# Kernel tuning notes

Hardware: AMD Instinct MI355X
Metric: run time of the kernel (lower is better)

## Reference

```python
import jax, jax.numpy as jnp
import numpy as np

G, K_ORD = 5, 3          # efficient-kan defaults: grid_size=5, spline_order=3
NB = G + K_ORD           # 8 spline basis functions per input feature
H, NH, S, B = 1024, 16, 1024, 2
HD = H // NH
DFF, E, TOPK = 1024, 4, 2


def b_splines(x):
    # x: [..., in] -> bases: [..., in, NB]; uniform grid on [-1,1] extended by K_ORD knots
    h = 2.0 / G
    grid = jnp.arange(-K_ORD, G + K_ORD + 1, dtype=x.dtype) * h - 1.0  # [G+2k+1]=12
    xg = x[..., None]
    bases = ((xg >= grid[:-1]) & (xg < grid[1:])).astype(x.dtype)      # order-0
    for j in range(1, K_ORD + 1):  # Cox-de Boor recursion
        left = (xg - grid[:-(j + 1)]) / (grid[j:-1] - grid[:-(j + 1)]) * bases[..., :-1]
        right = (grid[j + 1:] - xg) / (grid[j + 1:] - grid[1:-j]) * bases[..., 1:]
        bases = left + right
    return bases  # [..., in, NB]


def kan_linear(x, base_w, spline_w, scaler):
    # base path: SiLU(x) @ W_base^T ; spline path: B(x) contracted with scaled spline weights
    base = jax.nn.silu(x) @ base_w.T                       # [..., out]
    sw = spline_w * scaler[..., None]                      # [out, in, NB]
    spline = jnp.einsum('...ic,oic->...o', b_splines(x), sw)
    return base + spline


def rmsnorm(x, w, eps=1e-6):
    return w * (x * jax.lax.rsqrt(jnp.mean(x * x, axis=-1, keepdims=True) + eps))


def ffn(x, b1, s1, c1, b2, s2, c2, b3, s3, c3):
    # linear3(linear1(x) * linear2(x)), all KANLinear
    return kan_linear(kan_linear(x, b1, s1, c1) * kan_linear(x, b2, s2, c2), b3, s3, c3)


def setup_inputs() -> dict:
    key = jax.random.key(0)
    ks = jax.random.split(key, 24)
    sc = 0.02
    d = {}
    d['x'] = jax.random.normal(ks[0], (B, S, H), jnp.float32)
    inv_freq = 1.0 / (10000.0 ** (np.arange(0, HD, 2, dtype=np.float32) / HD))
    ang = np.arange(S, dtype=np.float32)[:, None] * inv_freq[None, :]  # [S, HD//2]
    d['rot_cos'] = jnp.asarray(np.cos(ang))
    d['rot_sin'] = jnp.asarray(np.sin(ang))
    d['norm1_w'] = jnp.ones((H,), jnp.float32)
    d['norm2_w'] = jnp.ones((H,), jnp.float32)
    d['qkv_base'] = jax.random.normal(ks[1], (3 * H, H), jnp.float32) * sc
    d['qkv_spline'] = jax.random.normal(ks[2], (3 * H, H, NB), jnp.float32) * sc
    d['qkv_scaler'] = jax.random.normal(ks[3], (3 * H, H), jnp.float32) * sc + 1.0
    d['out_w'] = jax.random.normal(ks[4], (H, H), jnp.float32) * sc
    d['out_b'] = jnp.zeros((H,), jnp.float32)
    d['gate_w'] = jax.random.normal(ks[5], (E, H), jnp.float32) * sc
    # stacked expert params (vmapped over E)
    d['w1_base'] = jax.random.normal(ks[6], (E, DFF, H), jnp.float32) * sc
    d['w1_spline'] = jax.random.normal(ks[7], (E, DFF, H, NB), jnp.float32) * sc
    d['w1_scaler'] = jax.random.normal(ks[8], (E, DFF, H), jnp.float32) * sc + 1.0
    d['w2_base'] = jax.random.normal(ks[9], (E, DFF, H), jnp.float32) * sc
    d['w2_spline'] = jax.random.normal(ks[10], (E, DFF, H, NB), jnp.float32) * sc
    d['w2_scaler'] = jax.random.normal(ks[11], (E, DFF, H), jnp.float32) * sc + 1.0
    d['w3_base'] = jax.random.normal(ks[12], (E, H, DFF), jnp.float32) * sc
    d['w3_spline'] = jax.random.normal(ks[13], (E, H, DFF, NB), jnp.float32) * sc
    d['w3_scaler'] = jax.random.normal(ks[14], (E, H, DFF), jnp.float32) * sc + 1.0
    return d


def reference(x, rot_cos, rot_sin, norm1_w, norm2_w, qkv_base, qkv_spline, qkv_scaler,
              out_w, out_b, gate_w, w1_base, w1_spline, w1_scaler, w2_base, w2_spline,
              w2_scaler, w3_base, w3_spline, w3_scaler):
    b, s, h = x.shape
    # ---- attention branch ----
    hn = rmsnorm(x, norm1_w)
    qkv = kan_linear(hn, qkv_base, qkv_spline, qkv_scaler)          # [B,S,3H]
    qkv = qkv.reshape(b, s, NH, 3 * HD).transpose(0, 2, 1, 3)       # [B,NH,S,3HD]
    q, k, v = jnp.split(qkv, 3, axis=-1)                            # [B,NH,S,HD]

    def rope(t):
        tr = t.reshape(b, NH, s, HD // 2, 2)
        re, im = tr[..., 0], tr[..., 1]
        c, sn = rot_cos[:s], rot_sin[:s]                            # [S,HD//2]
        nre = re * c - im * sn
        nim = re * sn + im * c
        return jnp.stack([nre, nim], axis=-1).reshape(b, NH, s, HD)

    q, k = rope(q), rope(k)
    scores = jnp.einsum('bhqd,bhkd->bhqk', q, k) / (HD ** 0.5)
    attn = jax.nn.softmax(scores, axis=-1)
    ctx = jnp.einsum('bhqk,bhkd->bhqd', attn, v)
    ctx = ctx.transpose(0, 2, 1, 3).reshape(b, s, h)
    x = x + ctx @ out_w.T + out_b

    # ---- MoE-KAN FFN branch ----
    h2 = rmsnorm(x, norm2_w)
    gate_logits = h2 @ gate_w.T                                     # [B,S,E]
    w_top, sel = jax.lax.top_k(gate_logits, TOPK)                   # [B,S,K]
    w_top = jax.nn.softmax(w_top.astype(jnp.float32), axis=-1).astype(x.dtype)
    # run every expert densely (same math as masked dispatch), then gather top-k
    y_all = jax.vmap(
        lambda b1, s1, c1, b2, s2, c2, b3, s3, c3:
            ffn(h2, b1, s1, c1, b2, s2, c2, b3, s3, c3)
    )(w1_base, w1_spline, w1_scaler, w2_base, w2_spline, w2_scaler,
      w3_base, w3_spline, w3_scaler)                                # [E,B,S,H]
    y_bseh = jnp.transpose(y_all, (1, 2, 0, 3))                     # [B,S,E,H]
    gathered = jnp.take_along_axis(y_bseh, sel[..., None], axis=2)  # [B,S,K,H]
    moe_out = jnp.sum(w_top[..., None] * gathered, axis=2)          # [B,S,H]
    return x + moe_out
```

## Files before the change

### kernel.cpp

```cpp
#include <hip/hip_runtime.h>
#include <hip/hip_bf16.h>

#define T_TOK 2048
#define H_DIM 1024
#define S_SEQ 1024
#define NHEAD 16
#define E_EXP 4
#define DFF_  1024
#define KAUG  9216

typedef __bf16 bf16x8 __attribute__((ext_vector_type(8)));
typedef float  f32x4  __attribute__((ext_vector_type(4)));
typedef unsigned short ushort_t;

__device__ __forceinline__ float sigmoidf_(float x) { return 1.0f / (1.0f + __expf(-x)); }

__device__ __forceinline__ unsigned short f2bf(float f) {
    unsigned int u = __float_as_uint(f);
    u = (u + 0x7fffu + ((u >> 16) & 1u)) >> 16;
    return (unsigned short)u;
}
__device__ __forceinline__ float bf2f(unsigned short h) {
    return __uint_as_float(((unsigned int)h) << 16);
}

__device__ __forceinline__ void bspline8(float x, float* o) {
    float b[11];
#pragma unroll
    for (int m = 0; m < 11; ++m) {
        float g0 = 0.4f * (float)(m - 3) - 1.0f;
        float g1 = 0.4f * (float)(m - 2) - 1.0f;
        b[m] = (x >= g0 && x < g1) ? 1.0f : 0.0f;
    }
#pragma unroll
    for (int j = 1; j <= 3; ++j) {
        float inv = 1.0f / (0.4f * (float)j);
#pragma unroll
        for (int m = 0; m + j < 11; ++m) {
            float gm   = 0.4f * (float)(m - 3) - 1.0f;
            float gmj1 = 0.4f * (float)(m + j - 2) - 1.0f;
            b[m] = ((x - gm) * b[m] + (gmj1 - x) * b[m + 1]) * inv;
        }
    }
#pragma unroll
    for (int c = 0; c < 8; ++c) o[c] = b[c];
}

__global__ __launch_bounds__(256) void rmsnorm_kernel(const float* __restrict__ x,
                                                      const float* __restrict__ w,
                                                      float* __restrict__ out) {
    long t = blockIdx.x;
    float4 v = ((const float4*)(x + t * H_DIM))[threadIdx.x];
    float ss = v.x * v.x + v.y * v.y + v.z * v.z + v.w * v.w;
#pragma unroll
    for (int m = 1; m < 64; m <<= 1) ss += __shfl_xor(ss, m, 64);
    __shared__ float wsum[4];
    if ((threadIdx.x & 63) == 0) wsum[threadIdx.x >> 6] = ss;
    __syncthreads();
    ss = wsum[0] + wsum[1] + wsum[2] + wsum[3];
    float sc = rsqrtf(ss * (1.0f / (float)H_DIM) + 1e-6f);
    float4 wv = ((const float4*)w)[threadIdx.x];
    float4 r;
    r.x = v.x * sc * wv.x; r.y = v.y * sc * wv.y;
    r.z = v.z * sc * wv.z; r.w = v.w * sc * wv.w;
    ((float4*)(out + t * H_DIM))[threadIdx.x] = r;
}

__global__ __launch_bounds__(256) void prefill_out(const float* __restrict__ x,
                                                   const float* __restrict__ bias,
                                                   float* __restrict__ out) {
    long i = (long)blockIdx.x * 256 + threadIdx.x;
    float4 xv = ((const float4*)x)[i];
    float4 bv = ((const float4*)bias)[i & 255];
    float4 r;
    r.x = xv.x + bv.x; r.y = xv.y + bv.y; r.z = xv.z + bv.z; r.w = xv.w + bv.w;
    ((float4*)out)[i] = r;
}

__global__ __launch_bounds__(256) void pack_act(const float* __restrict__ act,
                                                ushort_t* __restrict__ hi,
                                                ushort_t* __restrict__ lo) {
    long idx = (long)blockIdx.x * 256 + threadIdx.x;
    long m = idx >> 10; int i = (int)(idx & 1023);
    float v = act[idx];
    float ch[9];
    ch[0] = v * sigmoidf_(v);
    bspline8(v, ch + 1);
    ushort_t* oh = hi + m * (long)KAUG + i;
#pragma unroll
    for (int c = 0; c < 9; ++c) oh[(long)c * 1024] = f2bf(ch[c]);
    if (lo) {
        ushort_t* ol = lo + m * (long)KAUG + i;
#pragma unroll
        for (int c = 0; c < 9; ++c) {
            unsigned short h = f2bf(ch[c]);
            ol[(long)c * 1024] = f2bf(ch[c] - bf2f(h));
        }
    }
}

__global__ __launch_bounds__(256) void pack_w(const float* __restrict__ base,
                                              const float* __restrict__ spl,
                                              const float* __restrict__ scal,
                                              ushort_t* __restrict__ hi,
                                              ushort_t* __restrict__ lo,
                                              long total) {
    long idx = (long)blockIdx.x * 256 + threadIdx.x;
    if (idx >= total) return;
    long n = idx >> 10; int i = (int)(idx & 1023);
    float sc = scal[idx];
    const float4* s4 = (const float4*)(spl + idx * 8);
    float4 s0 = s4[0], s1 = s4[1];
    float ch[9] = {base[idx], s0.x * sc, s0.y * sc, s0.z * sc, s0.w * sc,
                   s1.x * sc, s1.y * sc, s1.z * sc, s1.w * sc};
    ushort_t* oh = hi + n * (long)KAUG + i;
#pragma unroll
    for (int c = 0; c < 9; ++c) oh[(long)c * 1024] = f2bf(ch[c]);
    if (lo) {
        ushort_t* ol = lo + n * (long)KAUG + i;
#pragma unroll
        for (int c = 0; c < 9; ++c) {
            unsigned short h = f2bf(ch[c]);
            ol[(long)c * 1024] = f2bf(ch[c] - bf2f(h));
        }
    }
}

__global__ __launch_bounds__(256) void mul_pack4(const ushort_t* __restrict__ g12,
                                                 ushort_t* __restrict__ G) {
    long idx = (long)blockIdx.x * 256 + threadIdx.x;
    long t = idx >> 12; int ei = (int)(idx & 4095);
    int e = ei >> 10, i = ei & 1023;
    float g1 = bf2f(g12[t * 8192 + ei]);
    float g2 = bf2f(g12[t * 8192 + 4096 + ei]);
    float v = g1 * g2;
    float ch[9];
    ch[0] = v * sigmoidf_(v);
    bspline8(v, ch + 1);
    ushort_t* oh = G + ((long)e * T_TOK + t) * (long)KAUG + i;
#pragma unroll
    for (int c = 0; c < 9; ++c) oh[(long)c * 1024] = f2bf(ch[c]);
}

__global__ __launch_bounds__(256) void split_pack(const float* __restrict__ in,
                                                  ushort_t* __restrict__ hi,
                                                  ushort_t* __restrict__ lo, long n) {
    long i = (long)blockIdx.x * 256 + threadIdx.x;
    if (i >= n) return;
    float v = in[i];
    unsigned short h = f2bf(v);
    hi[i] = h;
    lo[i] = f2bf(v - bf2f(h));
}

#define GLD(gp, lp) __builtin_amdgcn_global_load_lds( \
    (const __attribute__((address_space(1))) void*)(gp), \
    (__attribute__((address_space(3))) void*)(lp), 16, 0, 0)

template<int BM, int SPLIT, int MODE, int KSPLIT>
__global__ __launch_bounds__(256) void mfma_gemm2(const ushort_t* __restrict__ Ah,
                                                  const ushort_t* __restrict__ Al,
                                                  const ushort_t* __restrict__ Bh,
                                                  const ushort_t* __restrict__ Bl,
                                                  float* __restrict__ C,
                                                  const float* __restrict__ rowScale,
                                                  int N, int K) {
    constexpr int NM = BM / 32;
    __shared__ __align__(16) ushort_t AsH[BM * 32];
    __shared__ __align__(16) ushort_t BsH[128 * 32];
    __shared__ __align__(16) ushort_t AsL[SPLIT ? BM * 32 : 16];
    __shared__ __align__(16) ushort_t BsL[SPLIT ? 128 * 32 : 16];
    const int bm = blockIdx.y * BM, bn = blockIdx.x * 128;

    const int KC = K / KSPLIT;
    int e = 0, kk = 0;
    if constexpr (MODE == 3) { e = blockIdx.z / KSPLIT; kk = blockIdx.z % KSPLIT; }
    else if constexpr (KSPLIT > 1) { kk = blockIdx.z; }
    const ushort_t* Ap = Ah + (MODE == 3 ? (size_t)e * (size_t)gridDim.y * BM * K : 0)
                            + (size_t)kk * KC;
    const ushort_t* Bp = Bh + (MODE == 3 ? (size_t)e * (size_t)N * K : 0)
                            + (size_t)kk * KC;
    const ushort_t* Alp = SPLIT ? Al + (size_t)kk * KC : nullptr;
    const ushort_t* Blp = SPLIT ? Bl + (size_t)kk * KC : nullptr;
    const float* rsp = rowScale + (MODE == 3 ? e : 0);

    const int tid = threadIdx.x;
    const int w = tid >> 6, l = tid & 63;
    const int wr = w >> 1, wc = w & 1;
    const int half = l >> 4, lr = l & 15;
    const size_t rb = (size_t)K * 2;

    const int rowB0 = w * 32 + (l >> 2), rowB1 = rowB0 + 16;
    const int cch = l & 3;
    const char* gB0 = (const char*)Bp + (size_t)(bn + rowB0) * rb + ((cch ^ (rowB0 & 3)) * 16);
    const char* gB1 = (const char*)Bp + (size_t)(bn + rowB1) * rb + ((cch ^ (rowB1 & 3)) * 16);
    const char* gB0l = SPLIT ? (const char*)Blp + (size_t)(bn + rowB0) * rb + ((cch ^ (rowB0 & 3)) * 16) : nullptr;
    const char* gB1l = SPLIT ? (const char*)Blp + (size_t)(bn + rowB1) * rb + ((cch ^ (rowB1 & 3)) * 16) : nullptr;
    int rowA0, rowA1;
    if constexpr (BM == 128) { rowA0 = w * 32 + (l >> 2); rowA1 = rowA0 + 16; }
    else                     { rowA0 = w * 16 + (l >> 2); rowA1 = 0; }
    const char* gA0 = (const char*)Ap + (size_t)(bm + rowA0) * rb + ((cch ^ (rowA0 & 3)) * 16);
    const char* gA1 = (BM == 128) ? (const char*)Ap + (size_t)(bm + rowA1) * rb + ((cch ^ (rowA1 & 3)) * 16) : nullptr;
    const char* gA0l = SPLIT ? (const char*)Alp + (size_t)(bm + rowA0) * rb + ((cch ^ (rowA0 & 3)) * 16) : nullptr;
    const char* gA1l = (SPLIT && BM == 128) ? (const char*)Alp + (size_t)(bm + rowA1) * rb + ((cch ^ (rowA1 & 3)) * 16) : nullptr;

    f32x4 acc[NM][4] = {};
    for (int k0 = 0; k0 < KC; k0 += 32) {
        const size_t kb = (size_t)k0 * 2;
        GLD(gA0 + kb, (char*)AsH + ((BM == 128) ? w * 2048 : w * 1024) + l * 16);
        if constexpr (BM == 128) GLD(gA1 + kb, (char*)AsH + w * 2048 + 1024 + l * 16);
        GLD(gB0 + kb, (char*)BsH + w * 2048 + l * 16);
        GLD(gB1 + kb, (char*)BsH + w * 2048 + 1024 + l * 16);
        if constexpr (SPLIT) {
            GLD(gA0l + kb, (char*)AsL + ((BM == 128) ? w * 2048 : w * 1024) + l * 16);
            if constexpr (BM == 128) GLD(gA1l + kb, (char*)AsL + w * 2048 + 1024 + l * 16);
            GLD(gB0l + kb, (char*)BsL + w * 2048 + l * 16);
            GLD(gB1l + kb, (char*)BsL + w * 2048 + 1024 + l * 16);
        }
        __syncthreads();
        bf16x8 ah[NM], bh[4];
#pragma unroll
        for (int mi = 0; mi < NM; ++mi) {
            int r = wr * (BM / 2) + mi * 16 + lr;
            ah[mi] = *(const bf16x8*)((const char*)AsH + r * 64 + ((half ^ (r & 3)) * 16));
        }
#pragma unroll
        for (int ni = 0; ni < 4; ++ni) {
            int r = wc * 64 + ni * 16 + lr;
            bh[ni] = *(const bf16x8*)((const char*)BsH + r * 64 + ((half ^ (r & 3)) * 16));
        }
#pragma unroll
        for (int mi = 0; mi < NM; ++mi)
#pragma unroll
            for (int ni = 0; ni < 4; ++ni)
                acc[mi][ni] = __builtin_amdgcn_mfma_f32_16x16x32_bf16(ah[mi], bh[ni],
                                                                      acc[mi][ni], 0, 0, 0);
        if constexpr (SPLIT) {
            bf16x8 al[NM], bl[4];
#pragma unroll
            for (int mi = 0; mi < NM; ++mi) {
                int r = wr * (BM / 2) + mi * 16 + lr;
                al[mi] = *(const bf16x8*)((const char*)AsL + r * 64 + ((half ^ (r & 3)) * 16));
            }
#pragma unroll
            for (int ni = 0; ni < 4; ++ni) {
                int r = wc * 64 + ni * 16 + lr;
                bl[ni] = *(const bf16x8*)((const char*)BsL + r * 64 + ((half ^ (r & 3)) * 16));
            }
#pragma unroll
            for (int mi = 0; mi < NM; ++mi)
#pragma unroll
                for (int ni = 0; ni < 4; ++ni) {
                    acc[mi][ni] = __builtin_amdgcn_mfma_f32_16x16x32_bf16(ah[mi], bl[ni],
                                                                          acc[mi][ni], 0, 0, 0);
                    acc[mi][ni] = __builtin_amdgcn_mfma_f32_16x16x32_bf16(al[mi], bh[ni],
                                                                          acc[mi][ni], 0, 0, 0);
                }
        }
        __syncthreads();
    }
#pragma unroll
    for (int mi = 0; mi < NM; ++mi)
#pragma unroll
        for (int r = 0; r < 4; ++r) {
            int row = bm + wr * (BM / 2) + mi * 16 + half * 4 + r;
            float rs = (MODE == 3) ? rsp[(size_t)row * 4] : 0.0f;
#pragma unroll
            for (int ni = 0; ni < 4; ++ni) {
                int col = bn + wc * 64 + ni * 16 + lr;
                size_t ix = (size_t)row * N + col;
                if constexpr (MODE == 0)      C[ix] = acc[mi][ni][r];
                else if constexpr (MODE == 3) unsafeAtomicAdd(&C[ix], rs * acc[mi][ni][r]);
                else if constexpr (MODE == 5) unsafeAtomicAdd(&C[ix], acc[mi][ni][r]);
                else                          ((ushort_t*)C)[ix] = f2bf(acc[mi][ni][r]);
            }
        }
}

__global__ __launch_bounds__(256) void qk_pack(const float* __restrict__ qkv,
                                               const float* __restrict__ cs,
                                               const float* __restrict__ sn,
                                               ushort_t* __restrict__ Qh, ushort_t* __restrict__ Ql,
                                               ushort_t* __restrict__ Kh, ushort_t* __restrict__ Kl) {
    int idx = blockIdx.x * 256 + threadIdx.x;
    int p = idx & 31;
    int h = (idx >> 5) & 15;
    int s = (idx >> 9) & (S_SEQ - 1);
    int b = idx >> 19;
    float c = cs[s * 32 + p], si = sn[s * 32 + p];
    long base = ((long)(b * S_SEQ + s)) * 3072 + h * 192;
    long dst = (((long)(b * NHEAD + h)) * S_SEQ + s) * 64 + 2 * p;
    float re = qkv[base + 2 * p], im = qkv[base + 2 * p + 1];
    float qre = (re * c - im * si) * 0.125f;
    float qim = (re * si + im * c) * 0.125f;
    unsigned short hh = f2bf(qre);
    Qh[dst] = hh; Ql[dst] = f2bf(qre - bf2f(hh));
    hh = f2bf(qim);
    Qh[dst + 1] = hh; Ql[dst + 1] = f2bf(qim - bf2f(hh));
    re = qkv[base + 64 + 2 * p]; im = qkv[base + 64 + 2 * p + 1];
    float kre = re * c - im * si;
    float kim = re * si + im * c;
    hh = f2bf(kre);
    Kh[dst] = hh; Kl[dst] = f2bf(kre - bf2f(hh));
    hh = f2bf(kim);
    Kh[dst + 1] = hh; Kl[dst + 1] = f2bf(kim - bf2f(hh));
}

__global__ __launch_bounds__(256) void v_trans(const float* __restrict__ qkv,
                                               ushort_t* __restrict__ Vth,
                                               ushort_t* __restrict__ Vtl) {
    __shared__ float t[64][65];
    const int s0 = blockIdx.x * 64, h = blockIdx.y, b = blockIdx.z;
    const int tid = threadIdx.x;
#pragma unroll
    for (int i = 0; i < 16; ++i) {
        int e = tid + i * 256;
        int sl = e >> 6, d = e & 63;
        t[d][sl] = qkv[((long)(b * S_SEQ + s0 + sl)) * 3072 + h * 192 + 128 + d];
    }
    __syncthreads();
#pragma unroll
    for (int i = 0; i < 16; ++i) {
        int e = tid + i * 256;
        int d = e >> 6, sl = e & 63;
        float v = t[d][sl];
        long o = (((long)(b * NHEAD + h)) * 64 + d) * S_SEQ + s0 + sl;
        unsigned short hh = f2bf(v);
        Vth[o] = hh;
        Vtl[o] = f2bf(v - bf2f(hh));
    }
}

__device__ __forceinline__ bf16x8 lds_frag(const ushort_t* base, int row, int chunk) {
    return *(const bf16x8*)((const char*)base + row * 128 + ((chunk ^ (row & 7)) * 16));
}

__global__ __launch_bounds__(256) void attn_mfma(const ushort_t* __restrict__ Qh,
                                                 const ushort_t* __restrict__ Ql,
                                                 const ushort_t* __restrict__ Kh,
                                                 const ushort_t* __restrict__ Kl,
                                                 const ushort_t* __restrict__ Vth,
                                                 const ushort_t* __restrict__ Vtl,
                                                 float* __restrict__ ctx) {
    __shared__ __align__(16) ushort_t KsH[64 * 64], KsL[64 * 64];
    __shared__ __align__(16) ushort_t VsH[64 * 64], VsL[64 * 64];
    __shared__ __align__(16) ushort_t Ps[4][2][16][72];
    const int qb = blockIdx.x * 64, h = blockIdx.y, b = blockIdx.z;
    const int tid = threadIdx.x;
    const int w = tid >> 6, l = tid & 63;
    const int lr = l & 15, g = l >> 4;
    const long bh = b * NHEAD + h;

    const long qoff = (bh * S_SEQ + qb + w * 16 + lr) * 64 + g * 8;
    bf16x8 qh0 = *(const bf16x8*)(Qh + qoff);
    bf16x8 qh1 = *(const bf16x8*)(Qh + qoff + 32);
    bf16x8 ql0 = *(const bf16x8*)(Ql + qoff);
    bf16x8 ql1 = *(const bf16x8*)(Ql + qoff + 32);

    const int rowS0 = w * 16 + (l >> 3), rowS1 = rowS0 + 8;
    const int cch = l & 7;
    const char* gK0 = (const char*)Kh + (bh * S_SEQ + rowS0) * 128 + ((cch ^ (rowS0 & 7)) * 16);
    const char* gK1 = (const char*)Kh + (bh * S_SEQ + rowS1) * 128 + ((cch ^ (rowS1 & 7)) * 16);
    const char* gKl0 = (const char*)Kl + (bh * S_SEQ + rowS0) * 128 + ((cch ^ (rowS0 & 7)) * 16);
    const char* gKl1 = (const char*)Kl + (bh * S_SEQ + rowS1) * 128 + ((cch ^ (rowS1 & 7)) * 16);
    const char* gV0 = (const char*)Vth + (bh * 64 + rowS0) * 2048 + ((cch ^ (rowS0 & 7)) * 16);
    const char* gV1 = (const char*)Vth + (bh * 64 + rowS1) * 2048 + ((cch ^ (rowS1 & 7)) * 16);
    const char* gVl0 = (const char*)Vtl + (bh * 64 + rowS0) * 2048 + ((cch ^ (rowS0 & 7)) * 16);
    const char* gVl1 = (const char*)Vtl + (bh * 64 + rowS1) * 2048 + ((cch ^ (rowS1 & 7)) * 16);

    float m_run[4] = {-1e30f, -1e30f, -1e30f, -1e30f};
    float l_run[4] = {0.f, 0.f, 0.f, 0.f};
    f32x4 acco[4] = {};

    for (int k0 = 0; k0 < S_SEQ; k0 += 64) {
        GLD(gK0 + (size_t)k0 * 128, (char*)KsH + w * 2048 + l * 16);
        GLD(gK1 + (size_t)k0 * 128, (char*)KsH + w * 2048 + 1024 + l * 16);
        GLD(gKl0 + (size_t)k0 * 128, (char*)KsL + w * 2048 + l * 16);
        GLD(gKl1 + (size_t)k0 * 128, (char*)KsL + w * 2048 + 1024 + l * 16);
        GLD(gV0 + (size_t)k0 * 2, (char*)VsH + w * 2048 + l * 16);
        GLD(gV1 + (size_t)k0 * 2, (char*)VsH + w * 2048 + 1024 + l * 16);
        GLD(gVl0 + (size_t)k0 * 2, (char*)VsL + w * 2048 + l * 16);
        GLD(gVl1 + (size_t)k0 * 2, (char*)VsL + w * 2048 + 1024 + l * 16);
        __syncthreads();

        f32x4 accs[4] = {};
#pragma unroll
        for (int n = 0; n < 4; ++n) {
            bf16x8 bkh0 = lds_frag(KsH, n * 16 + lr, g);
            bf16x8 bkh1 = lds_frag(KsH, n * 16 + lr, g + 4);
            bf16x8 bkl0 = lds_frag(KsL, n * 16 + lr, g);
            bf16x8 bkl1 = lds_frag(KsL, n * 16 + lr, g + 4);
            accs[n] = __builtin_amdgcn_mfma_f32_16x16x32_bf16(qh0, bkh0, accs[n], 0, 0, 0);
            accs[n] = __builtin_amdgcn_mfma_f32_16x16x32_bf16(qh1, bkh1, accs[n], 0, 0, 0);
            accs[n] = __builtin_amdgcn_mfma_f32_16x16x32_bf16(qh0, bkl0, accs[n], 0, 0, 0);
            accs[n] = __builtin_amdgcn_mfma_f32_16x16x32_bf16(qh1, bkl1, accs[n], 0, 0, 0);
            accs[n] = __builtin_amdgcn_mfma_f32_16x16x32_bf16(ql0, bkh0, accs[n], 0, 0, 0);
            accs[n] = __builtin_amdgcn_mfma_f32_16x16x32_bf16(ql1, bkh1, accs[n], 0, 0, 0);
        }
        float alpha[4];
#pragma unroll
        for (int r = 0; r < 4; ++r) {
            float mx = fmaxf(fmaxf(accs[0][r], accs[1][r]), fmaxf(accs[2][r], accs[3][r]));
#pragma unroll
            for (int msk = 1; msk < 16; msk <<= 1) mx = fmaxf(mx, __shfl_xor(mx, msk, 64));
            float m_new = fmaxf(m_run[r], mx);
            float ps = 0.f;
#pragma unroll
            for (int n = 0; n < 4; ++n) {
                float p = __expf(accs[n][r] - m_new);
                accs[n][r] = p;
                ps += p;
            }
#pragma unroll
            for (int msk = 1; msk < 16; msk <<= 1) ps += __shfl_xor(ps, msk, 64);
            alpha[r] = __expf(m_run[r] - m_new);
            l_run[r] = l_run[r] * alpha[r] + ps;
            m_run[r] = m_new;
        }
#pragma unroll
        for (int nd = 0; nd < 4; ++nd)
#pragma unroll
            for (int r = 0; r < 4; ++r) acco[nd][r] *= alpha[r];
#pragma unroll
        for (int n = 0; n < 4; ++n)
#pragma unroll
            for (int r = 0; r < 4; ++r) {
                float p = accs[n][r];
                unsigned short hh = f2bf(p);
                Ps[w][0][g * 4 + r][n * 16 + lr] = hh;
                Ps[w][1][g * 4 + r][n * 16 + lr] = f2bf(p - bf2f(hh));
            }
        __syncthreads();
        bf16x8 pah0 = *(const bf16x8*)&Ps[w][0][lr][g * 8];
        bf16x8 pah1 = *(const bf16x8*)&Ps[w][0][lr][32 + g * 8];
        bf16x8 pal0 = *(const bf16x8*)&Ps[w][1][lr][g * 8];
        bf16x8 pal1 = *(const bf16x8*)&Ps[w][1][lr][32 + g * 8];
#pragma unroll
        for (int nd = 0; nd < 4; ++nd) {
            bf16x8 bvh0 = lds_frag(VsH, nd * 16 + lr, g);
            bf16x8 bvh1 = lds_frag(VsH, nd * 16 + lr, g + 4);
            bf16x8 bvl0 = lds_frag(VsL, nd * 16 + lr, g);
            bf16x8 bvl1 = lds_frag(VsL, nd * 16 + lr, g + 4);
            acco[nd] = __builtin_amdgcn_mfma_f32_16x16x32_bf16(pah0, bvh0, acco[nd], 0, 0, 0);
            acco[nd] = __builtin_amdgcn_mfma_f32_16x16x32_bf16(pah1, bvh1, acco[nd], 0, 0, 0);
            acco[nd] = __builtin_amdgcn_mfma_f32_16x16x32_bf16(pah0, bvl0, acco[nd], 0, 0, 0);
            acco[nd] = __builtin_amdgcn_mfma_f32_16x16x32_bf16(pah1, bvl1, acco[nd], 0, 0, 0);
            acco[nd] = __builtin_amdgcn_mfma_f32_16x16x32_bf16(pal0, bvh0, acco[nd], 0, 0, 0);
            acco[nd] = __builtin_amdgcn_mfma_f32_16x16x32_bf16(pal1, bvh1, acco[nd], 0, 0, 0);
        }
        __syncthreads();
    }
#pragma unroll
    for (int r = 0; r < 4; ++r) {
        float inv = 1.0f / l_run[r];
        long row = (long)b * S_SEQ + qb + w * 16 + g * 4 + r;
#pragma unroll
        for (int nd = 0; nd < 4; ++nd)
            ctx[row * H_DIM + h * 64 + nd * 16 + lr] = acco[nd][r] * inv;
    }
}

__global__ __launch_bounds__(256) void gate_kernel(const float* __restrict__ h2,
                                                   const float* __restrict__ gate_w,
                                                   float* __restrict__ gw) {
    long t = blockIdx.x;
    float sum[4] = {0, 0, 0, 0};
    for (int i = threadIdx.x; i < H_DIM; i += 256) {
        float v = h2[t * H_DIM + i];
#pragma unroll
        for (int e = 0; e < 4; ++e) sum[e] = fmaf(v, gate_w[e * H_DIM + i], sum[e]);
    }
#pragma unroll
    for (int w = 1; w < 64; w <<= 1)
#pragma unroll
        for (int e = 0; e < 4; ++e) sum[e] += __shfl_xor(sum[e], w, 64);
    __shared__ float part[4][4];
    if ((threadIdx.x & 63) == 0)
#pragma unroll
        for (int e = 0; e < 4; ++e) part[e][threadIdx.x >> 6] = sum[e];
    __syncthreads();
    if (threadIdx.x == 0) {
        float lg[4];
#pragma unroll
        for (int e = 0; e < 4; ++e) lg[e] = part[e][0] + part[e][1] + part[e][2] + part[e][3];
        int i0 = 0;
        for (int e = 1; e < 4; ++e) if (lg[e] > lg[i0]) i0 = e;
        int i1 = -1;
        for (int e = 0; e < 4; ++e) if (e != i0 && (i1 < 0 || lg[e] > lg[i1])) i1 = e;
        float mx = fmaxf(lg[i0], lg[i1]);
        float e0 = __expf(lg[i0] - mx), e1 = __expf(lg[i1] - mx);
        float inv = 1.0f / (e0 + e1);
        float o[4] = {0, 0, 0, 0};
        o[i0] = e0 * inv; o[i1] = e1 * inv;
#pragma unroll
        for (int e = 0; e < 4; ++e) gw[t * 4 + e] = o[e];
    }
}

#define KI 8
#define BKK 72
__global__ __launch_bounds__(256) void kan_gemm(const float* __restrict__ Act,
                                                const float* __restrict__ baseW,
                                                const float* __restrict__ splW,
                                                const float* __restrict__ scal,
                                                float* __restrict__ C,
                                                const float* __restrict__ rowScale,
                                                int rsStride, int N, int mode) {
    __shared__ float As[BKK][64];
    __shared__ float Bs[BKK][64];
    const int bm = blockIdx.y * 64;
    const int bn = blockIdx.x * 64;
    const int tid = threadIdx.x;
    const int tx = tid & 15, ty = tid >> 4;
    float acc[4][4] = {};
    for (int i0 = 0; i0 < H_DIM; i0 += KI) {
        for (int e = tid; e < 64 * KI; e += 256) {
            int m = e >> 3, ii = e & 7;
            float xv = Act[(long)(bm + m) * H_DIM + i0 + ii];
            float sp[8];
            bspline8(xv, sp);
            As[ii * 9][m] = xv * sigmoidf_(xv);
#pragma unroll
            for (int c = 0; c < 8; ++c) As[ii * 9 + 1 + c][m] = sp[c];
        }
        for (int e = tid; e < 64 * KI; e += 256) {
            int n = e >> 3, ii = e & 7;
            long w = (long)(bn + n) * H_DIM + i0 + ii;
            float sc = scal[w];
            Bs[ii * 9][n] = baseW[w];
            const float4* sp4 = (const float4*)(splW + w * 8);
            float4 s0 = sp4[0], s1 = sp4[1];
            Bs[ii * 9 + 1][n] = s0.x * sc; Bs[ii * 9 + 2][n] = s0.y * sc;
            Bs[ii * 9 + 3][n] = s0.z * sc; Bs[ii * 9 + 4][n] = s0.w * sc;
            Bs[ii * 9 + 5][n] = s1.x * sc; Bs[ii * 9 + 6][n] = s1.y * sc;
            Bs[ii * 9 + 7][n] = s1.z * sc; Bs[ii * 9 + 8][n] = s1.w * sc;
        }
        __syncthreads();
#pragma unroll 8
        for (int k = 0; k < BKK; ++k) {
            float4 a = *(const float4*)&As[k][ty * 4];
            float4 b = *(const float4*)&Bs[k][tx * 4];
            float av[4] = {a.x, a.y, a.z, a.w};
            float bv[4] = {b.x, b.y, b.z, b.w};
#pragma unroll
            for (int i = 0; i < 4; ++i)
#pragma unroll
                for (int j = 0; j < 4; ++j) acc[i][j] = fmaf(av[i], bv[j], acc[i][j]);
        }
        __syncthreads();
    }
#pragma unroll
    for (int i = 0; i < 4; ++i) {
        long m = bm + ty * 4 + i;
        float rs = (mode == 1) ? rowScale[m * rsStride] : 0.0f;
#pragma unroll
        for (int j = 0; j < 4; ++j) {
            long idx = m * (long)N + bn + tx * 4 + j;
            if (mode == 0) C[idx] = acc[i][j];
            else           C[idx] += rs * acc[i][j];
        }
    }
}

__global__ __launch_bounds__(256) void gemm_bias_res(const float* __restrict__ A,
                                                     const float* __restrict__ Bw,
                                                     const float* __restrict__ bias,
                                                     const float* __restrict__ res,
                                                     float* __restrict__ C) {
    __shared__ float As[16][64];
    __shared__ float Bs[16][64];
    const int bm = blockIdx.y * 64, bn = blockIdx.x * 64;
    const int tid = threadIdx.x;
    const int tx = tid & 15, ty = tid >> 4;
    float acc[4][4] = {};
    for (int k0 = 0; k0 < 1024; k0 += 16) {
        for (int e = tid; e < 1024; e += 256) {
            int r = e >> 4, kk = e & 15;
            As[kk][r] = A[(long)(bm + r) * 1024 + k0 + kk];
            Bs[kk][r] = Bw[(long)(bn + r) * 1024 + k0 + kk];
        }
        __syncthreads();
#pragma unroll
        for (int k = 0; k < 16; ++k) {
            float4 a = *(const float4*)&As[k][ty * 4];
            float4 b = *(const float4*)&Bs[k][tx * 4];
            float av[4] = {a.x, a.y, a.z, a.w};
            float bv[4] = {b.x, b.y, b.z, b.w};
#pragma unroll
            for (int i = 0; i < 4; ++i)
#pragma unroll
                for (int j = 0; j < 4; ++j) acc[i][j] = fmaf(av[i], bv[j], acc[i][j]);
        }
        __syncthreads();
    }
#pragma unroll
    for (int i = 0; i < 4; ++i) {
        long m = bm + ty * 4 + i;
#pragma unroll
        for (int j = 0; j < 4; ++j) {
            long n = bn + tx * 4 + j;
            C[m * 1024 + n] = res[m * 1024 + n] + bias[n] + acc[i][j];
        }
    }
}

__global__ __launch_bounds__(256) void rope_kernel(float* __restrict__ qkv,
                                                   const float* __restrict__ cs,
                                                   const float* __restrict__ sn) {
    int idx = blockIdx.x * 256 + threadIdx.x;
    if (idx >= T_TOK * NHEAD * 32) return;
    int p = idx & 31;
    int n = (idx >> 5) & 15;
    int t = idx >> 9;
    int s = t & (S_SEQ - 1);
    float c = cs[s * 32 + p], si = sn[s * 32 + p];
    long base = (long)t * 3072 + n * 192;
    float re = qkv[base + 2 * p], im = qkv[base + 2 * p + 1];
    qkv[base + 2 * p]     = re * c - im * si;
    qkv[base + 2 * p + 1] = re * si + im * c;
    re = qkv[base + 64 + 2 * p]; im = qkv[base + 64 + 2 * p + 1];
    qkv[base + 64 + 2 * p]     = re * c - im * si;
    qkv[base + 64 + 2 * p + 1] = re * si + im * c;
}

__global__ __launch_bounds__(256) void attn_kernel(const float* __restrict__ qkv,
                                                   float* __restrict__ ctx) {
    const int qb = blockIdx.x * 32;
    const int h = blockIdx.y, b = blockIdx.z;
    __shared__ float Qs[32][64];
    __shared__ float Ks[64][64];
    __shared__ float Vs[64][64];
    __shared__ float Ss[32][64];
    const int tid = threadIdx.x;
    const int q = tid >> 3, g = tid & 7;
    for (int e = tid; e < 32 * 64; e += 256) {
        int r = e >> 6, d = e & 63;
        Qs[r][d] = qkv[(long)(b * S_SEQ + qb + r) * 3072 + h * 192 + d];
    }
    float m_run = -1e30f, l_run = 0.0f;
    float acc[8] = {};
    for (int k0 = 0; k0 < S_SEQ; k0 += 64) {
        for (int e = tid; e < 64 * 64; e += 256) {
            int r = e >> 6, d = e & 63;
            long base = (long)(b * S_SEQ + k0 + r) * 3072 + h * 192;
            Ks[r][d] = qkv[base + 64 + d];
            Vs[r][d] = qkv[base + 128 + d];
        }
        __syncthreads();
        float s[8];
#pragma unroll
        for (int kk = 0; kk < 8; ++kk) {
            int k = g * 8 + kk;
            float dot = 0.0f;
#pragma unroll
            for (int d = 0; d < 64; ++d) dot = fmaf(Qs[q][d], Ks[k][d], dot);
            s[kk] = dot * 0.125f;
        }
        float mx = s[0];
#pragma unroll
        for (int kk = 1; kk < 8; ++kk) mx = fmaxf(mx, s[kk]);
#pragma unroll
        for (int w = 1; w < 8; w <<= 1) mx = fmaxf(mx, __shfl_xor(mx, w, 64));
        float m_new = fmaxf(m_run, mx);
        float p[8], ls = 0.0f;
#pragma unroll
        for (int kk = 0; kk < 8; ++kk) { p[kk] = __expf(s[kk] - m_new); ls += p[kk]; }
#pragma unroll
        for (int w = 1; w < 8; w <<= 1) ls += __shfl_xor(ls, w, 64);
        float alpha = __expf(m_run - m_new);
        l_run = l_run * alpha + ls;
        m_run = m_new;
#pragma unroll
        for (int kk = 0; kk < 8; ++kk) Ss[q][g * 8 + kk] = p[kk];
        __syncthreads();
#pragma unroll
        for (int j = 0; j < 8; ++j) acc[j] *= alpha;
        for (int k = 0; k < 64; ++k) {
            float pv = Ss[q][k];
#pragma unroll
            for (int j = 0; j < 8; ++j) acc[j] = fmaf(pv, Vs[k][g * 8 + j], acc[j]);
        }
        __syncthreads();
    }
    float inv = 1.0f / l_run;
#pragma unroll
    for (int j = 0; j < 8; ++j)
        ctx[(long)(b * S_SEQ + qb + q) * H_DIM + h * 64 + g * 8 + j] = acc[j] * inv;
}

__global__ __launch_bounds__(256) void mul_kernel(const float* __restrict__ a,
                                                  const float* __restrict__ b,
                                                  float* __restrict__ c, int n) {
    int i = blockIdx.x * 256 + threadIdx.x;
    if (i < n) c[i] = a[i] * b[i];
}

extern "C" void kernel_launch(void* const* d_in, const int* in_sizes, int n_in,
                              void* d_out, int out_size, void* d_ws, size_t ws_size,
                              hipStream_t stream) {
    const float* x          = (const float*)d_in[0];
    const float* rot_cos    = (const float*)d_in[1];
    const float* rot_sin    = (const float*)d_in[2];
    const float* norm1_w    = (const float*)d_in[3];
    const float* norm2_w    = (const float*)d_in[4];
    const float* qkv_base   = (const float*)d_in[5];
    const float* qkv_spline = (const float*)d_in[6];
    const float* qkv_scaler = (const float*)d_in[7];
    const float* out_w      = (const float*)d_in[8];
    const float* out_b      = (const float*)d_in[9];
    const float* gate_w     = (const float*)d_in[10];
    const float* w1_base    = (const float*)d_in[11];
    const float* w1_spline  = (const float*)d_in[12];
    const float* w1_scaler  = (const float*)d_in[13];
    const float* w2_base    = (const float*)d_in[14];
    const float* w2_spline  = (const float*)d_in[15];
    const float* w2_scaler  = (const float*)d_in[16];
    const float* w3_base    = (const float*)d_in[17];
    const float* w3_spline  = (const float*)d_in[18];
    const float* w3_scaler  = (const float*)d_in[19];
    float* out = (float*)d_out;

    const size_t SZ_AUG  = (size_t)T_TOK * KAUG * 2;
    const size_t SZ_WQ   = (size_t)3072 * KAUG * 2;
    const size_t SZ_QKV  = (size_t)T_TOK * 3072 * 4;
    const size_t SZ_G12  = (size_t)T_TOK * 2048 * 4;
    const size_t SZ_TOK  = (size_t)T_TOK * H_DIM * 4;
    const size_t NEED = 2 * SZ_AUG + 2 * SZ_WQ + SZ_QKV + SZ_G12 + 2 * SZ_TOK + 32768;

    if (ws_size >= NEED) {
        char* pool = (char*)d_ws;
        ushort_t* A_hi = (ushort_t*)pool;
        ushort_t* A_lo = (ushort_t*)(pool + SZ_AUG);
        char* W1p = pool + 2 * SZ_AUG;
        char* W2p = pool + 2 * SZ_AUG + SZ_WQ;
        float* qkv = (float*)(pool + 2 * SZ_AUG + 2 * SZ_WQ);
        float* ctx = (float*)(pool + 2 * SZ_AUG + 2 * SZ_WQ + SZ_QKV + SZ_G12);
        float* tok = (float*)(pool + 2 * SZ_AUG + 2 * SZ_WQ + SZ_QKV + SZ_G12 + SZ_TOK);
        float* gw  = (float*)(pool + NEED - 32768);
        ushort_t* W1b = (ushort_t*)W1p;
        ushort_t* W2b = (ushort_t*)W2p;
        const size_t SZ_P = (size_t)T_TOK * 1024 * 2;
        ushort_t* Qh  = (ushort_t*)W1p;
        ushort_t* Ql  = (ushort_t*)(W1p + SZ_P);
        ushort_t* Kh  = (ushort_t*)(W1p + 2 * SZ_P);
        ushort_t* Kl  = (ushort_t*)(W1p + 3 * SZ_P);
        ushort_t* Vth = (ushort_t*)(W1p + 4 * SZ_P);
        ushort_t* Vtl = (ushort_t*)(W1p + 5 * SZ_P);
        ushort_t* CtxH = (ushort_t*)W2p;
        ushort_t* CtxL = (ushort_t*)(W2p + SZ_P);
        ushort_t* OWh  = (ushort_t*)(W2p + 2 * SZ_P);
        ushort_t* OWl  = (ushort_t*)(W2p + 2 * SZ_P + SZ_P / 2);
        const size_t SZ_W12 = (size_t)8192 * KAUG * 2;
        ushort_t* A2   = (ushort_t*)pool;
        ushort_t* W12  = (ushort_t*)(pool + SZ_AUG);
        ushort_t* g12  = (ushort_t*)(pool + SZ_AUG + SZ_W12);
        ushort_t* Gall = (ushort_t*)pool;
        ushort_t* W3a  = (ushort_t*)(pool + 4 * SZ_AUG);

        rmsnorm_kernel<<<T_TOK, 256, 0, stream>>>(x, norm1_w, tok);
        pack_act<<<(T_TOK * 1024) / 256, 256, 0, stream>>>(tok, A_hi, A_lo);
        pack_w<<<(3072 * 1024) / 256, 256, 0, stream>>>(qkv_base, qkv_spline, qkv_scaler,
                                                        W1b, W2b, (long)3072 * 1024);
        hipMemsetAsync(qkv, 0, SZ_QKV, stream);
        mfma_gemm2<128, 1, 5, 4><<<dim3(3072 / 128, T_TOK / 128, 4), 256, 0, stream>>>(
            A_hi, A_lo, W1b, W2b, qkv, nullptr, 3072, KAUG);
        qk_pack<<<(T_TOK * NHEAD * 32) / 256, 256, 0, stream>>>(qkv, rot_cos, rot_sin,
                                                                Qh, Ql, Kh, Kl);
        v_trans<<<dim3(S_SEQ / 64, NHEAD, 2), 256, 0, stream>>>(qkv, Vth, Vtl);
        attn_mfma<<<dim3(S_SEQ / 64, NHEAD, 2), 256, 0, stream>>>(Qh, Ql, Kh, Kl,
                                                                  Vth, Vtl, ctx);
        split_pack<<<(T_TOK * 1024) / 256, 256, 0, stream>>>(ctx, CtxH, CtxL,
                                                             (long)T_TOK * 1024);
        split_pack<<<(1024 * 1024) / 256, 256, 0, stream>>>(out_w, OWh, OWl,
                                                            (long)1024 * 1024);
        prefill_out<<<(T_TOK * H_DIM / 4) / 256, 256, 0, stream>>>(x, out_b, out);
        mfma_gemm2<128, 1, 5, 4><<<dim3(1024 / 128, T_TOK / 128, 4), 256, 0, stream>>>(
            CtxH, CtxL, OWh, OWl, out, nullptr, 1024, 1024);
        rmsnorm_kernel<<<T_TOK, 256, 0, stream>>>(out, norm2_w, tok);
        gate_kernel<<<T_TOK, 256, 0, stream>>>(tok, gate_w, gw);

        pack_act<<<(T_TOK * 1024) / 256, 256, 0, stream>>>(tok, A2, nullptr);
        pack_w<<<(4 * 1024 * 1024) / 256, 256, 0, stream>>>(
            w1_base, w1_spline, w1_scaler, W12, nullptr, (long)4 * 1024 * 1024);
        pack_w<<<(4 * 1024 * 1024) / 256, 256, 0, stream>>>(
            w2_base, w2_spline, w2_scaler, W12 + (size_t)4096 * KAUG, nullptr,
            (long)4 * 1024 * 1024);
        mfma_gemm2<128, 0, 6, 1><<<dim3(8192 / 128, T_TOK / 128), 256, 0, stream>>>(
            A2, nullptr, W12, nullptr, (float*)g12, nullptr, 8192, KAUG);
        mul_pack4<<<(T_TOK * 4096) / 256, 256, 0, stream>>>(g12, Gall);
        pack_w<<<(4 * 1024 * 1024) / 256, 256, 0, stream>>>(
            w3_base, w3_spline, w3_scaler, W3a, nullptr, (long)4 * 1024 * 1024);
        mfma_gemm2<128, 0, 3, 2><<<dim3(1024 / 128, T_TOK / 128, E_EXP * 2), 256, 0, stream>>>(
            Gall, nullptr, W3a, nullptr, out, gw, 1024, KAUG);
        return;
    }

    char* ws = (char*)d_ws;
    float* hn  = (float*)ws; ws += (size_t)T_TOK * H_DIM * 4;
    float* qkv = (float*)ws; ws += (size_t)T_TOK * 3072 * 4;
    float* ctx = (float*)ws; ws += (size_t)T_TOK * H_DIM * 4;
    float* h2  = (float*)ws; ws += (size_t)T_TOK * H_DIM * 4;
    float* gw  = (float*)ws; ws += (size_t)T_TOK * E_EXP * 4;
    float* g1  = (float*)ws; ws += (size_t)T_TOK * DFF_ * 4;
    float* g2  = (float*)ws; ws += (size_t)T_TOK * DFF_ * 4;
    float* gm  = (float*)ws; ws += (size_t)T_TOK * DFF_ * 4;

    rmsnorm_kernel<<<T_TOK, 256, 0, stream>>>(x, norm1_w, hn);
    dim3 gq(3072 / 64, T_TOK / 64);
    kan_gemm<<<gq, 256, 0, stream>>>(hn, qkv_base, qkv_spline, qkv_scaler, qkv,
                                     nullptr, 0, 3072, 0);
    rope_kernel<<<(T_TOK * NHEAD * 32) / 256, 256, 0, stream>>>(qkv, rot_cos, rot_sin);
    dim3 ga(S_SEQ / 32, NHEAD, 2);
    attn_kernel<<<ga, 256, 0, stream>>>(qkv, ctx);
    dim3 go(1024 / 64, T_TOK / 64);
    gemm_bias_res<<<go, 256, 0, stream>>>(ctx, out_w, out_b, x, out);
    rmsnorm_kernel<<<T_TOK, 256, 0, stream>>>(out, norm2_w, h2);
    gate_kernel<<<T_TOK, 256, 0, stream>>>(h2, gate_w, gw);
    dim3 ge(1024 / 64, T_TOK / 64);
    for (int e = 0; e < E_EXP; ++e) {
        long wo = (long)e * DFF_ * H_DIM;
        kan_gemm<<<ge, 256, 0, stream>>>(h2, w1_base + wo, w1_spline + wo * 8,
                                         w1_scaler + wo, g1, nullptr, 0, DFF_, 0);
        kan_gemm<<<ge, 256, 0, stream>>>(h2, w2_base + wo, w2_spline + wo * 8,
                                         w2_scaler + wo, g2, nullptr, 0, DFF_, 0);
        mul_kernel<<<(T_TOK * DFF_) / 256, 256, 0, stream>>>(g1, g2, gm, T_TOK * DFF_);
        kan_gemm<<<ge, 256, 0, stream>>>(gm, w3_base + wo, w3_spline + wo * 8,
                                         w3_scaler + wo, out, gw + e, E_EXP, H_DIM, 1);
    }
}
```

Measured before the change: 1.490 ms.

## Replace dense all-expert MoE compute with top-k routed grouped GEMMs

Computes gating with top-2 selection, counts tokens per expert, builds a padded per-expert row map, and scatters token indices and weights. The expert W1/W2 GEMM then gathers only routed token rows per expert block, and the W3 GEMM scatters weighted results back with atomics. This removes the dense evaluation of all four experts for every token, roughly halving MoE FLOPs, at the cost of extra routing kernels, memsets, and indirect row loads. Padding rows map to token 0 with zero weight.

```diff
diff --git a/kernel.cpp b/kernel.cpp
--- a/kernel.cpp
+++ b/kernel.cpp
@@ -8,6 +8,8 @@
 #define E_EXP 4
 #define DFF_  1024
 #define KAUG  9216
+#define MROWS 4608
+#define NRB   36
 
 typedef __bf16 bf16x8 __attribute__((ext_vector_type(8)));
 typedef float  f32x4  __attribute__((ext_vector_type(4)));
@@ -126,18 +128,33 @@
     }
 }
 
-__global__ __launch_bounds__(256) void mul_pack4(const ushort_t* __restrict__ g12,
-                                                 ushort_t* __restrict__ G) {
+__global__ __launch_bounds__(256) void pack_w_g(const float* __restrict__ base,
+                                                const float* __restrict__ spl,
+                                                const float* __restrict__ scal,
+                                                ushort_t* __restrict__ hi,
+                                                int grpOff) {
     long idx = (long)blockIdx.x * 256 + threadIdx.x;
-    long t = idx >> 12; int ei = (int)(idx & 4095);
-    int e = ei >> 10, i = ei & 1023;
-    float g1 = bf2f(g12[t * 8192 + ei]);
-    float g2 = bf2f(g12[t * 8192 + 4096 + ei]);
-    float v = g1 * g2;
+    long n = idx >> 10; int i = (int)(idx & 1023);
+    long e = n >> 10, d = n & 1023;
+    float sc = scal[idx];
+    const float4* s4 = (const float4*)(spl + idx * 8);
+    float4 s0 = s4[0], s1 = s4[1];
+    float ch[9] = {base[idx], s0.x * sc, s0.y * sc, s0.z * sc, s0.w * sc,
+                   s1.x * sc, s1.y * sc, s1.z * sc, s1.w * sc};
+    ushort_t* oh = hi + (e * 2048 + grpOff + d) * (long)KAUG + i;
+#pragma unroll
+    for (int c = 0; c < 9; ++c) oh[(long)c * 1024] = f2bf(ch[c]);
+}
+
+__global__ __launch_bounds__(256) void mul_pack_g(const ushort_t* __restrict__ g12,
+                                                  ushort_t* __restrict__ G) {
+    long idx = (long)blockIdx.x * 256 + threadIdx.x;
+    long p = idx >> 10; int i = (int)(idx & 1023);
+    float v = bf2f(g12[p * 2048 + i]) * bf2f(g12[p * 2048 + 1024 + i]);
     float ch[9];
     ch[0] = v * sigmoidf_(v);
     bspline8(v, ch + 1);
-    ushort_t* oh = G + ((long)e * T_TOK + t) * (long)KAUG + i;
+    ushort_t* oh = G + p * (long)KAUG + i;
 #pragma unroll
     for (int c = 0; c < 9; ++c) oh[(long)c * 1024] = f2bf(ch[c]);
 }
@@ -163,7 +180,9 @@
                                                   const ushort_t* __restrict__ Bh,
                                                   const ushort_t* __restrict__ Bl,
                                                   float* __restrict__ C,
-                                                  const float* __restrict__ rowScale,
+                                                  const int* __restrict__ rmap,
+                                                  const int* __restrict__ eblk,
+                                                  const float* __restrict__ rwgt,
                                                   int N, int K) {
     constexpr int NM = BM / 32;
     __shared__ __align__(16) ushort_t AsH[BM * 32];
@@ -173,16 +192,15 @@
     const int bm = blockIdx.y * BM, bn = blockIdx.x * 128;
 
     const int KC = K / KSPLIT;
-    int e = 0, kk = 0;
-    if constexpr (MODE == 3) { e = blockIdx.z / KSPLIT; kk = blockIdx.z % KSPLIT; }
-    else if constexpr (KSPLIT > 1) { kk = blockIdx.z; }
-    const ushort_t* Ap = Ah + (MODE == 3 ? (size_t)e * (size_t)gridDim.y * BM * K : 0)
-                            + (size_t)kk * KC;
-    const ushort_t* Bp = Bh + (MODE == 3 ? (size_t)e * (size_t)N * K : 0)
-                            + (size_t)kk * KC;
+    int kk = (KSPLIT > 1) ? blockIdx.z : 0;
+    int e = 0;
+    if constexpr (MODE == 7 || MODE == 8) e = eblk[blockIdx.y];
+    const ushort_t* Ap = Ah + (size_t)kk * KC;
+    const ushort_t* Bp = Bh + (size_t)kk * KC
+                            + (MODE == 7 ? (size_t)e * 2048 * (size_t)K : 0)
+                            + (MODE == 8 ? (size_t)e * 1024 * (size_t)K : 0);
     const ushort_t* Alp = SPLIT ? Al + (size_t)kk * KC : nullptr;
     const ushort_t* Blp = SPLIT ? Bl + (size_t)kk * KC : nullptr;
-    const float* rsp = rowScale + (MODE == 3 ? e : 0);
 
     const int tid = threadIdx.x;
     const int w = tid >> 6, l = tid & 63;
@@ -199,10 +217,18 @@
     int rowA0, rowA1;
     if constexpr (BM == 128) { rowA0 = w * 32 + (l >> 2); rowA1 = rowA0 + 16; }
     else                     { rowA0 = w * 16 + (l >> 2); rowA1 = 0; }
-    const char* gA0 = (const char*)Ap + (size_t)(bm + rowA0) * rb + ((cch ^ (rowA0 & 3)) * 16);
-    const char* gA1 = (BM == 128) ? (const char*)Ap + (size_t)(bm + rowA1) * rb + ((cch ^ (rowA1 & 3)) * 16) : nullptr;
-    const char* gA0l = SPLIT ? (const char*)Alp + (size_t)(bm + rowA0) * rb + ((cch ^ (rowA0 & 3)) * 16) : nullptr;
-    const char* gA1l = (SPLIT && BM == 128) ? (const char*)Alp + (size_t)(bm + rowA1) * rb + ((cch ^ (rowA1 & 3)) * 16) : nullptr;
+    size_t arow0, arow1 = 0;
+    if constexpr (MODE == 7) {
+        arow0 = (size_t)rmap[bm + rowA0];
+        if (BM == 128) arow1 = (size_t)rmap[bm + rowA1];
+    } else {
+        arow0 = (size_t)(bm + rowA0);
+        if (BM == 128) arow1 = (size_t)(bm + rowA1);
+    }
+    const char* gA0 = (const char*)Ap + arow0 * rb + ((cch ^ (rowA0 & 3)) * 16);
+    const char* gA1 = (BM == 128) ? (const char*)Ap + arow1 * rb + ((cch ^ (rowA1 & 3)) * 16) : nullptr;
+    const char* gA0l = SPLIT ? (const char*)Alp + arow0 * rb + ((cch ^ (rowA0 & 3)) * 16) : nullptr;
+    const char* gA1l = (SPLIT && BM == 128) ? (const char*)Alp + arow1 * rb + ((cch ^ (rowA1 & 3)) * 16) : nullptr;
 
     f32x4 acc[NM][4] = {};
     for (int k0 = 0; k0 < KC; k0 += 32) {
@@ -264,14 +290,16 @@
 #pragma unroll
         for (int r = 0; r < 4; ++r) {
             int row = bm + wr * (BM / 2) + mi * 16 + half * 4 + r;
-            float rs = (MODE == 3) ? rsp[(size_t)row * 4] : 0.0f;
+            int token = 0; float wv = 0.0f;
+            if constexpr (MODE == 8) { token = rmap[row]; wv = rwgt[row]; }
 #pragma unroll
             for (int ni = 0; ni < 4; ++ni) {
                 int col = bn + wc * 64 + ni * 16 + lr;
                 size_t ix = (size_t)row * N + col;
                 if constexpr (MODE == 0)      C[ix] = acc[mi][ni][r];
-                else if constexpr (MODE == 3) unsafeAtomicAdd(&C[ix], rs * acc[mi][ni][r]);
                 else if constexpr (MODE == 5) unsafeAtomicAdd(&C[ix], acc[mi][ni][r]);
+                else if constexpr (MODE == 8)
+                    unsafeAtomicAdd(&C[(size_t)token * N + col], wv * acc[mi][ni][r]);
                 else                          ((ushort_t*)C)[ix] = f2bf(acc[mi][ni][r]);
             }
         }
@@ -460,9 +488,11 @@
     }
 }
 
-__global__ __launch_bounds__(256) void gate_kernel(const float* __restrict__ h2,
-                                                   const float* __restrict__ gate_w,
-                                                   float* __restrict__ gw) {
+__global__ __launch_bounds__(256) void gate_route(const float* __restrict__ h2,
+                                                  const float* __restrict__ gate_w,
+                                                  int2* __restrict__ sel,
+                                                  float2* __restrict__ selw,
+                                                  int* __restrict__ cnts) {
     long t = blockIdx.x;
     float sum[4] = {0, 0, 0, 0};
     for (int i = threadIdx.x; i < H_DIM; i += 256) {
@@ -490,11 +520,41 @@
         float mx = fmaxf(lg[i0], lg[i1]);
         float e0 = __expf(lg[i0] - mx), e1 = __expf(lg[i1] - mx);
         float inv = 1.0f / (e0 + e1);
-        float o[4] = {0, 0, 0, 0};
-        o[i0] = e0 * inv; o[i1] = e1 * inv;
-#pragma unroll
-        for (int e = 0; e < 4; ++e) gw[t * 4 + e] = o[e];
-    }
+        sel[t] = make_int2(i0, i1);
+        selw[t] = make_float2(e0 * inv, e1 * inv);
+        atomicAdd(&cnts[i0], 1);
+        atomicAdd(&cnts[i1], 1);
+    }
+}
+
+__global__ void route_offsets(const int* __restrict__ cnts, int* __restrict__ fill,
+                              int* __restrict__ off, int* __restrict__ eblk) {
+    if (threadIdx.x != 0) return;
+    int o = 0;
+    for (int e = 0; e < 4; ++e) {
+        off[e] = o;
+        fill[e] = o;
+        o += ((cnts[e] + 127) >> 7) << 7;
+    }
+    off[4] = o;
+    for (int rb = 0; rb < NRB; ++rb) {
+        int rs = rb * 128, e = 0;
+        for (int q = 0; q < 4; ++q)
+            if (rs >= off[q] && rs < off[q + 1]) e = q;
+        eblk[rb] = e;
+    }
+}
+
+__global__ __launch_bounds__(256) void route_scatter(const int2* __restrict__ sel,
+                                                     const float2* __restrict__ selw,
+                                                     int* __restrict__ fill,
+                                                     int* __restrict__ map,
+                                                     float* __restrict__ wgt) {
+    int t = blockIdx.x * 256 + threadIdx.x;
+    if (t >= T_TOK) return;
+    int2 s = sel[t]; float2 w = selw[t];
+    int p0 = atomicAdd(&fill[s.x], 1); map[p0] = t; wgt[p0] = w.x;
+    int p1 = atomicAdd(&fill[s.y], 1); map[p1] = t; wgt[p1] = w.y;
 }
 
 #define KI 8
@@ -686,6 +746,43 @@
 #pragma unroll
     for (int j = 0; j < 8; ++j)
         ctx[(long)(b * S_SEQ + qb + q) * H_DIM + h * 64 + g * 8 + j] = acc[j] * inv;
+}
+
+__global__ __launch_bounds__(256) void gate_kernel(const float* __restrict__ h2,
+                                                   const float* __restrict__ gate_w,
+                                                   float* __restrict__ gw) {
+    long t = blockIdx.x;
+    float sum[4] = {0, 0, 0, 0};
+    for (int i = threadIdx.x; i < H_DIM; i += 256) {
+        float v = h2[t * H_DIM + i];
+#pragma unroll
+        for (int e = 0; e < 4; ++e) sum[e] = fmaf(v, gate_w[e * H_DIM + i], sum[e]);
+    }
+#pragma unroll
+    for (int w = 1; w < 64; w <<= 1)
+#pragma unroll
+        for (int e = 0; e < 4; ++e) sum[e] += __shfl_xor(sum[e], w, 64);
+    __shared__ float part[4][4];
+    if ((threadIdx.x & 63) == 0)
+#pragma unroll
+        for (int e = 0; e < 4; ++e) part[e][threadIdx.x >> 6] = sum[e];
+    __syncthreads();
+    if (threadIdx.x == 0) {
+        float lg[4];
+#pragma unroll
+        for (int e = 0; e < 4; ++e) lg[e] = part[e][0] + part[e][1] + part[e][2] + part[e][3];
+        int i0 = 0;
+        for (int e = 1; e < 4; ++e) if (lg[e] > lg[i0]) i0 = e;
+        int i1 = -1;
+        for (int e = 0; e < 4; ++e) if (e != i0 && (i1 < 0 || lg[e] > lg[i1])) i1 = e;
+        float mx = fmaxf(lg[i0], lg[i1]);
+        float e0 = __expf(lg[i0] - mx), e1 = __expf(lg[i1] - mx);
+        float inv = 1.0f / (e0 + e1);
+        float o[4] = {0, 0, 0, 0};
+        o[i0] = e0 * inv; o[i1] = e1 * inv;
+#pragma unroll
+        for (int e = 0; e < 4; ++e) gw[t * 4 + e] = o[e];
+    }
 }
 
 __global__ __launch_bounds__(256) void mul_kernel(const float* __restrict__ a,
@@ -736,7 +833,6 @@
         float* qkv = (float*)(pool + 2 * SZ_AUG + 2 * SZ_WQ);
         float* ctx = (float*)(pool + 2 * SZ_AUG + 2 * SZ_WQ + SZ_QKV + SZ_G12);
         float* tok = (float*)(pool + 2 * SZ_AUG + 2 * SZ_WQ + SZ_QKV + SZ_G12 + SZ_TOK);
-        float* gw  = (float*)(pool + NEED - 32768);
         ushort_t* W1b = (ushort_t*)W1p;
         ushort_t* W2b = (ushort_t*)W2p;
         const size_t SZ_P = (size_t)T_TOK * 1024 * 2;
@@ -750,12 +846,23 @@
         ushort_t* CtxL = (ushort_t*)(W2p + SZ_P);
         ushort_t* OWh  = (ushort_t*)(W2p + 2 * SZ_P);
         ushort_t* OWl  = (ushort_t*)(W2p + 2 * SZ_P + SZ_P / 2);
-        const size_t SZ_W12 = (size_t)8192 * KAUG * 2;
+        const size_t SZ_W12G = (size_t)8192 * KAUG * 2;
+        const size_t SZ_G12G = (size_t)MROWS * 2048 * 2;
+        const size_t SZ_GG   = (size_t)MROWS * KAUG * 2;
         ushort_t* A2   = (ushort_t*)pool;
-        ushort_t* W12  = (ushort_t*)(pool + SZ_AUG);
-        ushort_t* g12  = (ushort_t*)(pool + SZ_AUG + SZ_W12);
-        ushort_t* Gall = (ushort_t*)pool;
-        ushort_t* W3a  = (ushort_t*)(pool + 4 * SZ_AUG);
+        ushort_t* W12g = (ushort_t*)(pool + SZ_AUG);
+        ushort_t* g12g = (ushort_t*)(pool + SZ_AUG + SZ_W12G);
+        char* route    = pool + SZ_AUG + SZ_W12G + SZ_G12G;
+        int2*   sel  = (int2*)route;
+        float2* selw = (float2*)(route + 16384);
+        int*    rmap = (int*)(route + 32768);
+        float*  rwgt = (float*)(route + 51200);
+        int*    cnts = (int*)(route + 69632);
+        int*    fill = cnts + 4;
+        int*    roff = cnts + 8;
+        int*    eblk = cnts + 16;
+        ushort_t* Gg  = (ushort_t*)pool;
+        ushort_t* W3a = (ushort_t*)(pool + SZ_GG);
 
         rmsnorm_kernel<<<T_TOK, 256, 0, stream>>>(x, norm1_w, tok);
         pack_act<<<(T_TOK * 1024) / 256, 256, 0, stream>>>(tok, A_hi, A_lo);
@@ -763,7 +870,7 @@
                                                         W1b, W2b, (long)3072 * 1024);
         hipMemsetAsync(qkv, 0, SZ_QKV, stream);
         mfma_gemm2<128, 1, 5, 4><<<dim3(3072 / 128, T_TOK / 128, 4), 256, 0, stream>>>(
-            A_hi, A_lo, W1b, W2b, qkv, nullptr, 3072, KAUG);
+            A_hi, A_lo, W1b, W2b, qkv, nullptr, nullptr, nullptr, 3072, KAUG);
         qk_pack<<<(T_TOK * NHEAD * 32) / 256, 256, 0, stream>>>(qkv, rot_cos, rot_sin,
                                                                 Qh, Ql, Kh, Kl);
         v_trans<<<dim3(S_SEQ / 64, NHEAD, 2), 256, 0, stream>>>(qkv, Vth, Vtl);
@@ -775,23 +882,27 @@
                                                             (long)1024 * 1024);
         prefill_out<<<(T_TOK * H_DIM / 4) / 256, 256, 0, stream>>>(x, out_b, out);
         mfma_gemm2<128, 1, 5, 4><<<dim3(1024 / 128, T_TOK / 128, 4), 256, 0, stream>>>(
-            CtxH, CtxL, OWh, OWl, out, nullptr, 1024, 1024);
+            CtxH, CtxL, OWh, OWl, out, nullptr, nullptr, nullptr, 1024, 1024);
         rmsnorm_kernel<<<T_TOK, 256, 0, stream>>>(out, norm2_w, tok);
-        gate_kernel<<<T_TOK, 256, 0, stream>>>(tok, gate_w, gw);
+
+        hipMemsetAsync(route + 32768, 0, 36864, stream);
+        hipMemsetAsync(cnts, 0, 256, stream);
+        gate_route<<<T_TOK, 256, 0, stream>>>(tok, gate_w, sel, selw, cnts);
+        route_offsets<<<1, 64, 0, stream>>>(cnts, fill, roff, eblk);
+        route_scatter<<<T_TOK / 256, 256, 0, stream>>>(sel, selw, fill, rmap, rwgt);
 
         pack_act<<<(T_TOK * 1024) / 256, 256, 0, stream>>>(tok, A2, nullptr);
-        pack_w<<<(4 * 1024 * 1024) / 256, 256, 0, stream>>>(
-            w1_base, w1_spline, w1_scaler, W12, nullptr, (long)4 * 1024 * 1024);
-        pack_w<<<(4 * 1024 * 1024) / 256, 256, 0, stream>>>(
-            w2_base, w2_spline, w2_scaler, W12 + (size_t)4096 * KAUG, nullptr,
-            (long)4 * 1024 * 1024);
-        mfma_gemm2<128, 0, 6, 1><<<dim3(8192 / 128, T_TOK / 128), 256, 0, stream>>>(
-            A2, nullptr, W12, nullptr, (float*)g12, nullptr, 8192, KAUG);
-        mul_pack4<<<(T_TOK * 4096) / 256, 256, 0, stream>>>(g12, Gall);
+        pack_w_g<<<(4 * 1024 * 1024) / 256, 256, 0, stream>>>(
+            w1_base, w1_spline, w1_scaler, W12g, 0);
+        pack_w_g<<<(4 * 1024 * 1024) / 256, 256, 0, stream>>>(
+            w2_base, w2_spline, w2_scaler, W12g, 1024);
+        mfma_gemm2<128, 0, 7, 1><<<dim3(2048 / 128, NRB), 256, 0, stream>>>(
+            A2, nullptr, W12g, nullptr, (float*)g12g, rmap, eblk, nullptr, 2048, KAUG);
+        mul_pack_g<<<(MROWS * 1024) / 256, 256, 0, stream>>>(g12g, Gg);
         pack_w<<<(4 * 1024 * 1024) / 256, 256, 0, stream>>>(
             w3_base, w3_spline, w3_scaler, W3a, nullptr, (long)4 * 1024 * 1024);
-        mfma_gemm2<128, 0, 3, 2><<<dim3(1024 / 128, T_TOK / 128, E_EXP * 2), 256, 0, stream>>>(
-            Gall, nullptr, W3a, nullptr, out, gw, 1024, KAUG);
+        mfma_gemm2<128, 0, 8, 2><<<dim3(1024 / 128, NRB, 2), 256, 0, stream>>>(
+            Gg, nullptr, W3a, nullptr, out, rmap, eblk, rwgt, 1024, KAUG);
         return;
     }
 
```

Measured after the change: 1.296 ms (median of 2 runs). 13.1% less time.
